# Kernel tuning notes

Measured on AMD Instinct MI355X. Metric: run time of the kernel, lower is better.

The kernel has to match this reference:

```python
import jax, jax.numpy as jnp
import numpy as np


def setup_inputs() -> dict:
    key = jax.random.key(0)
    k1, k2, k3, k4 = jax.random.split(key, 4)
    B, C, T, H, W = 2, 64, 8, 48, 48
    C2 = C // 2
    x_in = jax.random.normal(k1, (B, C, T, H, W), dtype=jnp.float32)
    # per-time-slice 1x1 conv weights (theta/phi pairs), kaiming-ish scale
    theta_w = jax.random.normal(k2, (T, C2, C), dtype=jnp.float32) / np.sqrt(C)
    phi_w = jax.random.normal(k3, (T, C2, C), dtype=jnp.float32) / np.sqrt(C)
    out_w = jax.random.normal(k4, (C, C), dtype=jnp.float32) / np.sqrt(C)
    return {"x_in": x_in, "theta_w": theta_w, "phi_w": phi_w, "out_w": out_w}


def reference(x_in, theta_w, phi_w, out_w):
    B, C, T, H, W = x_in.shape
    C2 = theta_w.shape[1]
    P = H * W
    # [B, T, C, P] layout: flatten spatial, move time next to batch
    x = jnp.transpose(x_in, (0, 2, 1, 3, 4)).reshape(B, T, C, P)
    # per-slice 1x1 convs == per-slice channel matmuls with slice-specific weights
    theta = jnp.einsum("toc,btcp->btop", theta_w, x)  # [B,T,C2,P]
    phi = jnp.einsum("toc,btcp->btop", phi_w, x)      # [B,T,C2,P]
    scale = 1.0 / jnp.sqrt(jnp.asarray(C2, dtype=x_in.dtype))
    scores = jnp.einsum("btcp,btcq->btpq", theta, phi) * scale  # [B,T,P,P]
    attn = jax.nn.softmax(scores, axis=-1)
    f = jnp.einsum("btpq,btcq->btcp", attn, x)  # value = raw x, [B,T,C,P]
    # conv_out: 1x1x1 Conv3d (pointwise over channels), then residual
    out = jnp.einsum("oc,btcp->btop", out_w, f)
    out = jnp.transpose(out.reshape(B, T, C, H, W), (0, 2, 1, 3, 4))
    return out + x_in
```

## Files before the change

kernel.cpp:

```cpp
#include <hip/hip_runtime.h>
#include <hip/hip_bf16.h>

#define CC 64
#define TT 8
#define PP 2304
#define C2 32
#define BT 16
#define NKT 36
#define SCALE2 0.25503486f

using h8 = __attribute__((ext_vector_type(8))) _Float16;
using h4 = __attribute__((ext_vector_type(4))) _Float16;
using f4 = __attribute__((ext_vector_type(4))) float;

#if __has_builtin(__builtin_amdgcn_exp2f)
#define EXP2(v) __builtin_amdgcn_exp2f(v)
#else
#define EXP2(v) exp2f(v)
#endif

#define SWIZ_BT(xcd, g) ((xcd) + 8 * ((g) & 1))
#define SWIZ_PT(g) ((g) >> 1)


__global__ __launch_bounds__(256) void k_prep(
    const float* __restrict__ x, const float* __restrict__ tw,
    const float* __restrict__ pw, _Float16* __restrict__ thf,
    _Float16* __restrict__ rec) {
  const int qt = SWIZ_PT(blockIdx.y), bt = SWIZ_BT(blockIdx.x, blockIdx.y);
  const int b = bt >> 3, t = bt & 7;
  const int tid = threadIdx.x;
  const int wv = tid >> 6, lane = tid & 63;
  const int quad = lane >> 4, l15 = lane & 15;

  __shared__ __align__(16) float x_s[64][68];
  __shared__ __align__(16) _Float16 th_s[4][16][32];
  __shared__ __align__(16) _Float16 ph_s[4][16][32];

  const size_t xslice = ((size_t)b * CC * TT + t) * PP;
  const int qg0 = qt * 64;

  {
    const int qq = tid & 63;
    const int c0 = (tid >> 6) * 16;
#pragma unroll
    for (int i = 0; i < 16; i++) {
      int c = c0 + i;
      x_s[qq][c] = x[xslice + (size_t)c * (TT * PP) + qg0 + qq];
    }
  }
  __syncthreads();

  h8 bx[2];
#pragma unroll
  for (int ks = 0; ks < 2; ks++) {
    const float* row = &x_s[wv * 16 + l15][ks * 32 + quad * 8];
    float4 u0 = *reinterpret_cast<const float4*>(row);
    float4 u1 = *reinterpret_cast<const float4*>(row + 4);
    bx[ks][0] = (_Float16)u0.x; bx[ks][1] = (_Float16)u0.y;
    bx[ks][2] = (_Float16)u0.z; bx[ks][3] = (_Float16)u0.w;
    bx[ks][4] = (_Float16)u1.x; bx[ks][5] = (_Float16)u1.y;
    bx[ks][6] = (_Float16)u1.z; bx[ks][7] = (_Float16)u1.w;
  }

  const float* twt = tw + t * C2 * CC;
  const float* pwt = pw + t * C2 * CC;
  const f4 zero = {0.f, 0.f, 0.f, 0.f};
  f4 accT[2] = {zero, zero}, accP[2] = {zero, zero};
#pragma unroll
  for (int mt = 0; mt < 2; mt++)
#pragma unroll
    for (int ks = 0; ks < 2; ks++) {
      const float* wr = twt + (mt * 16 + l15) * CC + ks * 32 + quad * 8;
      const float* pr = pwt + (mt * 16 + l15) * CC + ks * 32 + quad * 8;
      float4 a0 = *reinterpret_cast<const float4*>(wr);
      float4 a1 = *reinterpret_cast<const float4*>(wr + 4);
      float4 p0 = *reinterpret_cast<const float4*>(pr);
      float4 p1 = *reinterpret_cast<const float4*>(pr + 4);
      h8 at = {(_Float16)a0.x, (_Float16)a0.y, (_Float16)a0.z, (_Float16)a0.w,
               (_Float16)a1.x, (_Float16)a1.y, (_Float16)a1.z, (_Float16)a1.w};
      h8 ap = {(_Float16)p0.x, (_Float16)p0.y, (_Float16)p0.z, (_Float16)p0.w,
               (_Float16)p1.x, (_Float16)p1.y, (_Float16)p1.z, (_Float16)p1.w};
      accT[mt] =
          __builtin_amdgcn_mfma_f32_16x16x32_f16(at, bx[ks], accT[mt], 0, 0, 0);
      accP[mt] =
          __builtin_amdgcn_mfma_f32_16x16x32_f16(ap, bx[ks], accP[mt], 0, 0, 0);
    }

#pragma unroll
  for (int mt = 0; mt < 2; mt++) {
    h4 tv, pv;
#pragma unroll
    for (int r = 0; r < 4; r++) {
      tv[r] = (_Float16)(accT[mt][r] * SCALE2);
      pv[r] = (_Float16)accP[mt][r];
    }
    *reinterpret_cast<h4*>(&th_s[wv][l15][mt * 16 + quad * 4]) = tv;
    *reinterpret_cast<h4*>(&ph_s[wv][l15][mt * 16 + quad * 4]) = pv;
  }

  h8 tfrag = *reinterpret_cast<const h8*>(&th_s[wv][l15][quad * 8]);
  *reinterpret_cast<h8*>(
      thf + (((size_t)(bt * NKT + qt) * 4 + wv) * 64 + lane) * 8) = tfrag;

  _Float16* rb = rec + (size_t)(bt * NKT + qt) * 6144;
  h8 pfrag = *reinterpret_cast<const h8*>(&ph_s[wv][l15][quad * 8]);
  *reinterpret_cast<h8*>(rb + wv * 512 + lane * 8) = pfrag;

  {
    const int g = wv >> 1;
#pragma unroll
    for (int ct2 = 0; ct2 < 2; ct2++) {
      const int ct = (wv & 1) * 2 + ct2;
      h8 v;
#pragma unroll
      for (int j = 0; j < 4; j++) {
        v[j] = (_Float16)x_s[32 * g + quad * 4 + j][ct * 16 + l15];
        v[4 + j] = (_Float16)x_s[32 * g + 16 + quad * 4 + j][ct * 16 + l15];
      }
      *reinterpret_cast<h8*>(rb + 2048 + (g * 4 + ct) * 512 + lane * 8) = v;
    }
  }
}

__global__ __launch_bounds__(128, 2) void k_attn(
    const float* __restrict__ x, const _Float16* __restrict__ thf,
    const _Float16* __restrict__ rec, const float* __restrict__ ow,
    float* __restrict__ out) {
  const int pb = SWIZ_PT(blockIdx.y);
  const int bt = SWIZ_BT(blockIdx.x, blockIdx.y);
  const int b = bt >> 3, t = bt & 7;
  const int tid = threadIdx.x;
  const int wv = tid >> 6, lane = tid & 63;
  const int quad = lane >> 4, l15 = lane & 15;
  const int pstrip = pb * 2 + wv;

  const h8 bth0 = *reinterpret_cast<const h8*>(
      thf + (((size_t)bt * 144 + pstrip * 2 + 0) * 64 + lane) * 8);
  const h8 bth1 = *reinterpret_cast<const h8*>(
      thf + (((size_t)bt * 144 + pstrip * 2 + 1) * 64 + lane) * 8);

  const _Float16* recb = rec + (size_t)bt * NKT * 6144 + lane * 8;

  const f4 zero = {0.f, 0.f, 0.f, 0.f};
  f4 O[4][2];
#pragma unroll
  for (int ct = 0; ct < 4; ct++) {
    O[ct][0] = zero;
    O[ct][1] = zero;
  }
  float lsum[2] = {0.f, 0.f};

  h8 Abuf[12], Bbuf[12];

#define LOADREC(BUF, kt)                                          \
  {                                                               \
    const _Float16* _p = recb + (size_t)(kt)*6144;                \
    _Pragma("unroll") for (int j = 0; j < 12; j++)                \
        BUF[j] = *reinterpret_cast<const h8*>(_p + j * 512);      \
  }

#define COMPUTE(BUF)                                                          \
  {                                                                           \
    f4 s[2][4];                                                               \
    _Pragma("unroll") for (int pf = 0; pf < 2; pf++)                          \
        _Pragma("unroll") for (int nt = 0; nt < 4; nt++)                      \
            s[pf][nt] = __builtin_amdgcn_mfma_f32_16x16x32_f16(               \
                BUF[nt], pf ? bth1 : bth0, zero, 0, 0, 0);                    \
    _Pragma("unroll") for (int pf = 0; pf < 2; pf++)                          \
        _Pragma("unroll") for (int g = 0; g < 2; g++) {                       \
      h8 bw;                                                                  \
      _Pragma("unroll") for (int r = 0; r < 4; r++) {                         \
        float w0 = EXP2(s[pf][2 * g][r]);                                     \
        float w1 = EXP2(s[pf][2 * g + 1][r]);                                 \
        lsum[pf] += w0 + w1;                                                  \
        bw[r] = (_Float16)w0;                                                 \
        bw[4 + r] = (_Float16)w1;                                             \
      }                                                                       \
      _Pragma("unroll") for (int ct = 0; ct < 4; ct++)                        \
          O[ct][pf] = __builtin_amdgcn_mfma_f32_16x16x32_f16(                 \
              BUF[4 + g * 4 + ct], bw, O[ct][pf], 0, 0, 0);                   \
    }                                                                         \
  }

  LOADREC(Abuf, 0);
  for (int kt = 0; kt < NKT; kt += 2) {
    LOADREC(Bbuf, kt + 1);
    COMPUTE(Abuf);
    if (kt + 2 < NKT) LOADREC(Abuf, kt + 2);
    COMPUTE(Bbuf);
  }
#undef LOADREC
#undef COMPUTE

#pragma unroll
  for (int pf = 0; pf < 2; pf++) {
    lsum[pf] += __shfl_xor(lsum[pf], 16);
    lsum[pf] += __shfl_xor(lsum[pf], 32);
  }
  const float inv0 = 1.f / lsum[0], inv1 = 1.f / lsum[1];

  h4 bf[4][2];
#pragma unroll
  for (int ct = 0; ct < 4; ct++)
#pragma unroll
    for (int r = 0; r < 4; r++) {
      bf[ct][0][r] = (_Float16)(O[ct][0][r] * inv0);
      bf[ct][1][r] = (_Float16)(O[ct][1][r] * inv1);
    }

  f4 D3[4][2];
#pragma unroll
  for (int mt = 0; mt < 4; mt++) {
    D3[mt][0] = zero;
    D3[mt][1] = zero;
  }
#pragma unroll
  for (int mt = 0; mt < 4; mt++)
#pragma unroll
    for (int ct = 0; ct < 4; ct++) {
      const float* wrow =
          ow + (size_t)(mt * 16 + l15) * CC + ct * 16 + quad * 4;
      float4 u = *reinterpret_cast<const float4*>(wrow);
      h4 aw = {(_Float16)u.x, (_Float16)u.y, (_Float16)u.z, (_Float16)u.w};
      D3[mt][0] =
          __builtin_amdgcn_mfma_f32_16x16x16f16(aw, bf[ct][0], D3[mt][0], 0, 0, 0);
      D3[mt][1] =
          __builtin_amdgcn_mfma_f32_16x16x16f16(aw, bf[ct][1], D3[mt][1], 0, 0, 0);
    }

  const int p0g = pstrip * 32 + l15;
#pragma unroll
  for (int mt = 0; mt < 4; mt++)
#pragma unroll
    for (int r = 0; r < 4; r++) {
      const int o = mt * 16 + quad * 4 + r;
      const size_t base = ((size_t)(b * CC + o) * TT + t) * PP + p0g;
      out[base] = D3[mt][0][r] + x[base];
      out[base + 16] = D3[mt][1][r] + x[base + 16];
    }
}

extern "C" void kernel_launch(void* const* d_in, const int* in_sizes, int n_in,
                              void* d_out, int out_size, void* d_ws,
                              size_t ws_size, hipStream_t stream) {
  (void)in_sizes; (void)n_in; (void)out_size; (void)ws_size;
  const float* x = (const float*)d_in[0];
  const float* tw = (const float*)d_in[1];
  const float* pw = (const float*)d_in[2];
  const float* ow = (const float*)d_in[3];
  float* out = (float*)d_out;

  _Float16* thf = (_Float16*)d_ws;
  _Float16* rec = thf + (size_t)BT * NKT * 4 * 64 * 8;

  k_prep<<<dim3(8, 72), 256, 0, stream>>>(x, tw, pw, thf, rec);
  k_attn<<<dim3(8, 72), 128, 0, stream>>>(x, thf, rec, ow, out);
}
```

Before: 106.9 us.

## Split attention key range across two wave groups with LDS reduction

Doubles the attention block to 256 threads and has each pair of waves cover half of the key tiles (split-K), then combines partial outputs and row sums through shared memory before the output projection and residual write. This is meant to raise the number of waves and memory parallelism per query strip, shortening the serial loop over keys. In exchange it adds an LDS exchange, a barrier, and an epilogue where half the waves sit idle. Register pressure under launch bounds of 256 threads with 2 blocks per CU may also change.

```diff
diff --git a/kernel.cpp b/kernel.cpp
--- a/kernel.cpp
+++ b/kernel.cpp
@@ -7,6 +7,7 @@
 #define C2 32
 #define BT 16
 #define NKT 36
+#define HKT 18
 #define SCALE2 0.25503486f
 
 using h8 = __attribute__((ext_vector_type(8))) _Float16;
@@ -123,7 +124,7 @@
   }
 }
 
-__global__ __launch_bounds__(128, 2) void k_attn(
+__global__ __launch_bounds__(256, 2) void k_attn(
     const float* __restrict__ x, const _Float16* __restrict__ thf,
     const _Float16* __restrict__ rec, const float* __restrict__ ow,
     float* __restrict__ out) {
@@ -133,14 +134,18 @@
   const int tid = threadIdx.x;
   const int wv = tid >> 6, lane = tid & 63;
   const int quad = lane >> 4, l15 = lane & 15;
-  const int pstrip = pb * 2 + wv;
+  const int ps = wv & 1, kg = wv >> 1;
+  const int pstrip = pb * 2 + ps;
+
+  __shared__ float exch[2 * 35 * 64];
 
   const h8 bth0 = *reinterpret_cast<const h8*>(
       thf + (((size_t)bt * 144 + pstrip * 2 + 0) * 64 + lane) * 8);
   const h8 bth1 = *reinterpret_cast<const h8*>(
       thf + (((size_t)bt * 144 + pstrip * 2 + 1) * 64 + lane) * 8);
 
-  const _Float16* recb = rec + (size_t)bt * NKT * 6144 + lane * 8;
+  const _Float16* recb =
+      rec + ((size_t)bt * NKT + (size_t)kg * HKT) * 6144 + lane * 8;
 
   const f4 zero = {0.f, 0.f, 0.f, 0.f};
   f4 O[4][2];
@@ -184,10 +189,10 @@
   }
 
   LOADREC(Abuf, 0);
-  for (int kt = 0; kt < NKT; kt += 2) {
+  for (int kt = 0; kt < HKT; kt += 2) {
     LOADREC(Bbuf, kt + 1);
     COMPUTE(Abuf);
-    if (kt + 2 < NKT) LOADREC(Abuf, kt + 2);
+    if (kt + 2 < HKT) LOADREC(Abuf, kt + 2);
     COMPUTE(Bbuf);
   }
 #undef LOADREC
@@ -198,47 +203,63 @@
     lsum[pf] += __shfl_xor(lsum[pf], 16);
     lsum[pf] += __shfl_xor(lsum[pf], 32);
   }
-  const float inv0 = 1.f / lsum[0], inv1 = 1.f / lsum[1];
-
-  h4 bf[4][2];
-#pragma unroll
-  for (int ct = 0; ct < 4; ct++)
-#pragma unroll
-    for (int r = 0; r < 4; r++) {
-      bf[ct][0][r] = (_Float16)(O[ct][0][r] * inv0);
-      bf[ct][1][r] = (_Float16)(O[ct][1][r] * inv1);
-    }
-
-  f4 D3[4][2];
-#pragma unroll
-  for (int mt = 0; mt < 4; mt++) {
-    D3[mt][0] = zero;
-    D3[mt][1] = zero;
-  }
-#pragma unroll
-  for (int mt = 0; mt < 4; mt++)
-#pragma unroll
-    for (int ct = 0; ct < 4; ct++) {
-      const float* wrow =
-          ow + (size_t)(mt * 16 + l15) * CC + ct * 16 + quad * 4;
-      float4 u = *reinterpret_cast<const float4*>(wrow);
-      h4 aw = {(_Float16)u.x, (_Float16)u.y, (_Float16)u.z, (_Float16)u.w};
-      D3[mt][0] =
-          __builtin_amdgcn_mfma_f32_16x16x16f16(aw, bf[ct][0], D3[mt][0], 0, 0, 0);
-      D3[mt][1] =
-          __builtin_amdgcn_mfma_f32_16x16x16f16(aw, bf[ct][1], D3[mt][1], 0, 0, 0);
-    }
-
-  const int p0g = pstrip * 32 + l15;
-#pragma unroll
-  for (int mt = 0; mt < 4; mt++)
-#pragma unroll
-    for (int r = 0; r < 4; r++) {
-      const int o = mt * 16 + quad * 4 + r;
-      const size_t base = ((size_t)(b * CC + o) * TT + t) * PP + p0g;
-      out[base] = D3[mt][0][r] + x[base];
-      out[base + 16] = D3[mt][1][r] + x[base + 16];
-    }
+
+  if (kg == 1) {
+#pragma unroll
+    for (int k = 0; k < 32; k++)
+      exch[(ps * 35 + k) * 64 + lane] = O[k >> 3][(k >> 2) & 1][k & 3];
+    exch[(ps * 35 + 32) * 64 + lane] = lsum[0];
+    exch[(ps * 35 + 33) * 64 + lane] = lsum[1];
+  }
+  __syncthreads();
+
+  if (kg == 0) {
+#pragma unroll
+    for (int k = 0; k < 32; k++)
+      O[k >> 3][(k >> 2) & 1][k & 3] += exch[(ps * 35 + k) * 64 + lane];
+    const float inv0 = 1.f / (lsum[0] + exch[(ps * 35 + 32) * 64 + lane]);
+    const float inv1 = 1.f / (lsum[1] + exch[(ps * 35 + 33) * 64 + lane]);
+
+    h4 bf[4][2];
+#pragma unroll
+    for (int ct = 0; ct < 4; ct++)
+#pragma unroll
+      for (int r = 0; r < 4; r++) {
+        bf[ct][0][r] = (_Float16)(O[ct][0][r] * inv0);
+        bf[ct][1][r] = (_Float16)(O[ct][1][r] * inv1);
+      }
+
+    f4 D3[4][2];
+#pragma unroll
+    for (int mt = 0; mt < 4; mt++) {
+      D3[mt][0] = zero;
+      D3[mt][1] = zero;
+    }
+#pragma unroll
+    for (int mt = 0; mt < 4; mt++)
+#pragma unroll
+      for (int ct = 0; ct < 4; ct++) {
+        const float* wrow =
+            ow + (size_t)(mt * 16 + l15) * CC + ct * 16 + quad * 4;
+        float4 u = *reinterpret_cast<const float4*>(wrow);
+        h4 aw = {(_Float16)u.x, (_Float16)u.y, (_Float16)u.z, (_Float16)u.w};
+        D3[mt][0] = __builtin_amdgcn_mfma_f32_16x16x16f16(aw, bf[ct][0],
+                                                          D3[mt][0], 0, 0, 0);
+        D3[mt][1] = __builtin_amdgcn_mfma_f32_16x16x16f16(aw, bf[ct][1],
+                                                          D3[mt][1], 0, 0, 0);
+      }
+
+    const int p0g = pstrip * 32 + l15;
+#pragma unroll
+    for (int mt = 0; mt < 4; mt++)
+#pragma unroll
+      for (int r = 0; r < 4; r++) {
+        const int o = mt * 16 + quad * 4 + r;
+        const size_t base = ((size_t)(b * CC + o) * TT + t) * PP + p0g;
+        out[base] = D3[mt][0][r] + x[base];
+        out[base + 16] = D3[mt][1][r] + x[base + 16];
+      }
+  }
 }
 
 extern "C" void kernel_launch(void* const* d_in, const int* in_sizes, int n_in,
@@ -255,5 +276,5 @@
   _Float16* rec = thf + (size_t)BT * NKT * 4 * 64 * 8;
 
   k_prep<<<dim3(8, 72), 256, 0, stream>>>(x, tw, pw, thf, rec);
-  k_attn<<<dim3(8, 72), 128, 0, stream>>>(x, thf, rec, ow, out);
+  k_attn<<<dim3(8, 72), 256, 0, stream>>>(x, thf, rec, ow, out);
 }
```

Result: faster. 103.1 us (-3.5%).

## Split KV loop across four waves with LDS reduction and wider query tiles

Applied to the files above, without the earlier changes.

The attention kernel now uses 256-thread blocks. Each wave covers 64 query rows but only a quarter of the key tiles, so each wave's loaded key/value fragments are reused across more queries. This also doubles the number of resident waves available to hide latency. Partial numerators and softmax denominators are written to a 68 KB LDS buffer, reduced after a barrier, and each wave then finishes 16 rows through the output projection. Separately, the prep kernel's x load is vectorized to float4 reads with a transposed LDS store. The cost is the extra LDS exchange, a block-wide sync, and higher LDS pressure per block.

```diff
diff --git a/kernel.cpp b/kernel.cpp
--- a/kernel.cpp
+++ b/kernel.cpp
@@ -7,6 +7,7 @@
 #define C2 32
 #define BT 16
 #define NKT 36
+#define QKT 9
 #define SCALE2 0.25503486f
 
 using h8 = __attribute__((ext_vector_type(8))) _Float16;
@@ -41,12 +42,17 @@
   const int qg0 = qt * 64;
 
   {
-    const int qq = tid & 63;
-    const int c0 = (tid >> 6) * 16;
-#pragma unroll
-    for (int i = 0; i < 16; i++) {
-      int c = c0 + i;
-      x_s[qq][c] = x[xslice + (size_t)c * (TT * PP) + qg0 + qq];
+    const int l16 = tid & 15;
+    const int crow = tid >> 4;
+#pragma unroll
+    for (int ppass = 0; ppass < 4; ppass++) {
+      const int c = ppass * 16 + crow;
+      float4 u = *reinterpret_cast<const float4*>(
+          &x[xslice + (size_t)c * (TT * PP) + qg0 + l16 * 4]);
+      x_s[l16 * 4 + 0][c] = u.x;
+      x_s[l16 * 4 + 1][c] = u.y;
+      x_s[l16 * 4 + 2][c] = u.z;
+      x_s[l16 * 4 + 3][c] = u.w;
     }
   }
   __syncthreads();
@@ -123,33 +129,36 @@
   }
 }
 
-__global__ __launch_bounds__(128, 2) void k_attn(
+__global__ __launch_bounds__(256, 2) void k_attn(
     const float* __restrict__ x, const _Float16* __restrict__ thf,
     const _Float16* __restrict__ rec, const float* __restrict__ ow,
     float* __restrict__ out) {
-  const int pb = SWIZ_PT(blockIdx.y);
+  const int strip = SWIZ_PT(blockIdx.y);
   const int bt = SWIZ_BT(blockIdx.x, blockIdx.y);
   const int b = bt >> 3, t = bt & 7;
   const int tid = threadIdx.x;
-  const int wv = tid >> 6, lane = tid & 63;
+  const int kg = tid >> 6, lane = tid & 63;
   const int quad = lane >> 4, l15 = lane & 15;
-  const int pstrip = pb * 2 + wv;
-
-  const h8 bth0 = *reinterpret_cast<const h8*>(
-      thf + (((size_t)bt * 144 + pstrip * 2 + 0) * 64 + lane) * 8);
-  const h8 bth1 = *reinterpret_cast<const h8*>(
-      thf + (((size_t)bt * 144 + pstrip * 2 + 1) * 64 + lane) * 8);
-
-  const _Float16* recb = rec + (size_t)bt * NKT * 6144 + lane * 8;
+
+  __shared__ __align__(16) float exch[4 * 4 * 16 * 64];
+  __shared__ float exl[4 * 4 * 64];
+
+  h8 bth[4];
+#pragma unroll
+  for (int pf = 0; pf < 4; pf++)
+    bth[pf] = *reinterpret_cast<const h8*>(
+        thf + (((size_t)bt * 144 + strip * 4 + pf) * 64 + lane) * 8);
+
+  const _Float16* recb =
+      rec + ((size_t)bt * NKT + (size_t)kg * QKT) * 6144 + lane * 8;
 
   const f4 zero = {0.f, 0.f, 0.f, 0.f};
-  f4 O[4][2];
-#pragma unroll
-  for (int ct = 0; ct < 4; ct++) {
-    O[ct][0] = zero;
-    O[ct][1] = zero;
-  }
-  float lsum[2] = {0.f, 0.f};
+  f4 O[4][4];
+#pragma unroll
+  for (int ct = 0; ct < 4; ct++)
+#pragma unroll
+    for (int pf = 0; pf < 4; pf++) O[ct][pf] = zero;
+  float lsum[4] = {0.f, 0.f, 0.f, 0.f};
 
   h8 Abuf[12], Bbuf[12];
 
@@ -162,82 +171,92 @@
 
 #define COMPUTE(BUF)                                                          \
   {                                                                           \
-    f4 s[2][4];                                                               \
-    _Pragma("unroll") for (int pf = 0; pf < 2; pf++)                          \
-        _Pragma("unroll") for (int nt = 0; nt < 4; nt++)                      \
-            s[pf][nt] = __builtin_amdgcn_mfma_f32_16x16x32_f16(               \
-                BUF[nt], pf ? bth1 : bth0, zero, 0, 0, 0);                    \
-    _Pragma("unroll") for (int pf = 0; pf < 2; pf++)                          \
-        _Pragma("unroll") for (int g = 0; g < 2; g++) {                       \
-      h8 bw;                                                                  \
-      _Pragma("unroll") for (int r = 0; r < 4; r++) {                         \
-        float w0 = EXP2(s[pf][2 * g][r]);                                     \
-        float w1 = EXP2(s[pf][2 * g + 1][r]);                                 \
-        lsum[pf] += w0 + w1;                                                  \
-        bw[r] = (_Float16)w0;                                                 \
-        bw[4 + r] = (_Float16)w1;                                             \
+    _Pragma("unroll") for (int pf = 0; pf < 4; pf++) {                        \
+      f4 s[4];                                                                \
+      _Pragma("unroll") for (int nt = 0; nt < 4; nt++)                        \
+          s[nt] = __builtin_amdgcn_mfma_f32_16x16x32_f16(BUF[nt], bth[pf],    \
+                                                         zero, 0, 0, 0);     \
+      _Pragma("unroll") for (int g = 0; g < 2; g++) {                         \
+        h8 bw;                                                                \
+        _Pragma("unroll") for (int r = 0; r < 4; r++) {                       \
+          float w0 = EXP2(s[2 * g][r]);                                       \
+          float w1 = EXP2(s[2 * g + 1][r]);                                   \
+          lsum[pf] += w0 + w1;                                                \
+          bw[r] = (_Float16)w0;                                               \
+          bw[4 + r] = (_Float16)w1;                                           \
+        }                                                                     \
+        _Pragma("unroll") for (int ct = 0; ct < 4; ct++)                      \
+            O[ct][pf] = __builtin_amdgcn_mfma_f32_16x16x32_f16(               \
+                BUF[4 + g * 4 + ct], bw, O[ct][pf], 0, 0, 0);                 \
       }                                                                       \
-      _Pragma("unroll") for (int ct = 0; ct < 4; ct++)                        \
-          O[ct][pf] = __builtin_amdgcn_mfma_f32_16x16x32_f16(                 \
-              BUF[4 + g * 4 + ct], bw, O[ct][pf], 0, 0, 0);                   \
     }                                                                         \
   }
 
   LOADREC(Abuf, 0);
-  for (int kt = 0; kt < NKT; kt += 2) {
-    LOADREC(Bbuf, kt + 1);
+#pragma unroll 1
+  for (int i = 0; i < QKT - 1; i += 2) {
+    LOADREC(Bbuf, i + 1);
     COMPUTE(Abuf);
-    if (kt + 2 < NKT) LOADREC(Abuf, kt + 2);
+    LOADREC(Abuf, i + 2);
     COMPUTE(Bbuf);
   }
+  COMPUTE(Abuf);
 #undef LOADREC
 #undef COMPUTE
 
 #pragma unroll
-  for (int pf = 0; pf < 2; pf++) {
+  for (int pf = 0; pf < 4; pf++) {
     lsum[pf] += __shfl_xor(lsum[pf], 16);
     lsum[pf] += __shfl_xor(lsum[pf], 32);
   }
-  const float inv0 = 1.f / lsum[0], inv1 = 1.f / lsum[1];
-
-  h4 bf[4][2];
+
+#pragma unroll
+  for (int pf = 0; pf < 4; pf++) {
+#pragma unroll
+    for (int ct = 0; ct < 4; ct++)
+#pragma unroll
+      for (int r = 0; r < 4; r++)
+        exch[((kg * 4 + pf) * 16 + ct * 4 + r) * 64 + lane] = O[ct][pf][r];
+    exl[(kg * 4 + pf) * 64 + lane] = lsum[pf];
+  }
+  __syncthreads();
+
+  float ls = 0.f;
+#pragma unroll
+  for (int src = 0; src < 4; src++) ls += exl[(src * 4 + kg) * 64 + lane];
+  const float inv = 1.f / ls;
+
+  h4 bf[4];
 #pragma unroll
   for (int ct = 0; ct < 4; ct++)
 #pragma unroll
     for (int r = 0; r < 4; r++) {
-      bf[ct][0][r] = (_Float16)(O[ct][0][r] * inv0);
-      bf[ct][1][r] = (_Float16)(O[ct][1][r] * inv1);
-    }
-
-  f4 D3[4][2];
-#pragma unroll
-  for (int mt = 0; mt < 4; mt++) {
-    D3[mt][0] = zero;
-    D3[mt][1] = zero;
-  }
+      float acc = 0.f;
+#pragma unroll
+      for (int src = 0; src < 4; src++)
+        acc += exch[((src * 4 + kg) * 16 + ct * 4 + r) * 64 + lane];
+      bf[ct][r] = (_Float16)(acc * inv);
+    }
+
+  f4 D3[4] = {zero, zero, zero, zero};
 #pragma unroll
   for (int mt = 0; mt < 4; mt++)
 #pragma unroll
     for (int ct = 0; ct < 4; ct++) {
-      const float* wrow =
-          ow + (size_t)(mt * 16 + l15) * CC + ct * 16 + quad * 4;
+      const float* wrow = ow + (size_t)(mt * 16 + l15) * CC + ct * 16 + quad * 4;
       float4 u = *reinterpret_cast<const float4*>(wrow);
       h4 aw = {(_Float16)u.x, (_Float16)u.y, (_Float16)u.z, (_Float16)u.w};
-      D3[mt][0] =
-          __builtin_amdgcn_mfma_f32_16x16x16f16(aw, bf[ct][0], D3[mt][0], 0, 0, 0);
-      D3[mt][1] =
-          __builtin_amdgcn_mfma_f32_16x16x16f16(aw, bf[ct][1], D3[mt][1], 0, 0, 0);
-    }
-
-  const int p0g = pstrip * 32 + l15;
+      D3[mt] = __builtin_amdgcn_mfma_f32_16x16x16f16(aw, bf[ct], D3[mt], 0, 0, 0);
+    }
+
+  const int p0 = strip * 64 + kg * 16 + l15;
 #pragma unroll
   for (int mt = 0; mt < 4; mt++)
 #pragma unroll
     for (int r = 0; r < 4; r++) {
       const int o = mt * 16 + quad * 4 + r;
-      const size_t base = ((size_t)(b * CC + o) * TT + t) * PP + p0g;
-      out[base] = D3[mt][0][r] + x[base];
-      out[base + 16] = D3[mt][1][r] + x[base + 16];
+      const size_t base = ((size_t)(b * CC + o) * TT + t) * PP + p0;
+      out[base] = D3[mt][r] + x[base];
     }
 }
 
@@ -255,5 +274,5 @@
   _Float16* rec = thf + (size_t)BT * NKT * 4 * 64 * 8;
 
   k_prep<<<dim3(8, 72), 256, 0, stream>>>(x, tw, pw, thf, rec);
-  k_attn<<<dim3(8, 72), 128, 0, stream>>>(x, thf, rec, ow, out);
+  k_attn<<<dim3(8, 72), 256, 0, stream>>>(x, thf, rec, ow, out);
 }
```

Measured after the change: 104.7 us. 2.1% less time.
